# Performance work log

Measured on AMD Instinct MI355X. Metric: run time of the kernel, lower is better.

The kernel has to match this reference:

```python
import jax, jax.numpy as jnp
import numpy as np

DIM = 1024
E = 8
N = 4096
HID = 4 * DIM
THRESHOLD = 0.3


def setup_inputs() -> dict:
    key = jax.random.key(0)
    ks = jax.random.split(key, 8)
    s = 0.02
    return {
        "x": jax.random.normal(ks[0], (N, DIM), dtype=jnp.float32),
        "expert_inputs": jax.random.normal(ks[1], (E, N, DIM), dtype=jnp.float32),
        "wg": jax.random.normal(ks[2], (DIM, E), dtype=jnp.float32) * s,
        "bg": jnp.zeros((E,), dtype=jnp.float32),
        "w1": jax.random.normal(ks[3], (E, DIM, HID), dtype=jnp.float32) * s,
        "b1": jnp.zeros((E, HID), dtype=jnp.float32),
        "w2": jax.random.normal(ks[4], (E, HID, DIM), dtype=jnp.float32) * s,
        "b2": jnp.zeros((E, DIM), dtype=jnp.float32),
    }


def reference(x, expert_inputs, wg, bg, w1, b1, w2, b2):
    # Gate: softmax over experts. [N, E]
    gate_scores = jax.nn.softmax(x @ wg + bg, axis=-1)

    # Experts: FeedForward(dim, dim, mult=4) = Linear -> GELU -> Linear, batched over E.
    h = jax.nn.gelu(jnp.einsum('end,edh->enh', expert_inputs, w1) + b1[:, None, :],
                    approximate=False)  # [E, N, HID]
    expert_outputs = jnp.einsum('enh,ehd->end', h, w2) + b2[:, None, :]  # [E, N, D]
    expert_outputs = jnp.transpose(expert_outputs, (1, 0, 2))  # [N, E, D]

    # Threshold mask + renormalized weighted combine.
    mask = gate_scores >= THRESHOLD
    masked_scores = gate_scores * mask.astype(gate_scores.dtype)
    normed = masked_scores / (masked_scores.sum(axis=1, keepdims=True) + 1e-6)
    fused = jnp.einsum('ne,ned->nd', normed, expert_outputs)  # [N, D]

    # Fallback: rows with no expert above threshold take the top-1 expert output.
    top1 = jnp.argmax(gate_scores, axis=1)  # [N]
    fallback = jnp.take_along_axis(expert_outputs, top1[:, None, None], axis=1)[:, 0, :]
    fb_mask = (mask.sum(axis=1) == 0)[:, None]
    fused = jnp.where(fb_mask, fallback, fused)
    return fused, gate_scores
```

## Files before the change

### kernel.cpp

```cpp
#include <hip/hip_runtime.h>
#include <hip/hip_bf16.h>
#include <cstdint>

#define N_TOK 4096
#define DIM_  1024
#define HID_  4096
#define NEXP  8
#define HHALF 2048
#define CAP   (3 * N_TOK)

typedef __attribute__((ext_vector_type(8))) short short8;
typedef __attribute__((ext_vector_type(4))) float f32x4;

__device__ __forceinline__ unsigned short f32_to_bf16(float f) {
    union { float f; uint32_t u; } v;
    v.f = f;
    uint32_t r = (v.u + 0x7fffu + ((v.u >> 16) & 1u)) >> 16;
    return (unsigned short)r;
}

__device__ __forceinline__ float gelu_exact(float x) {
    return 0.5f * x * (1.0f + erff(x * 0.70710678118654752440f));
}

__device__ __forceinline__ void gl_lds16(const unsigned short* g, unsigned short* l) {
    __builtin_amdgcn_global_load_lds(
        (const __attribute__((address_space(1))) void*)g,
        (__attribute__((address_space(3))) void*)l, 16, 0, 0);
}

__global__ __launch_bounds__(256)
void zero_init_kernel(float* __restrict__ fused, int* __restrict__ cnt)
{
    const int b = blockIdx.x;
    if (b < N_TOK) {
        float4* p = (float4*)(fused + (size_t)b * DIM_);
        const int t = threadIdx.x;
        p[t] = make_float4(0.f, 0.f, 0.f, 0.f);
    } else if (threadIdx.x < NEXP) {
        cnt[threadIdx.x] = 0;
    }
}

__global__ __launch_bounds__(256)
void gate_kernel(const float* __restrict__ x, const float* __restrict__ wg,
                 const float* __restrict__ bg, float* __restrict__ gates,
                 float* __restrict__ wts, int* __restrict__ cnt)
{
    const int n = blockIdx.x;
    const int t = threadIdx.x;
    float acc[NEXP];
#pragma unroll
    for (int e = 0; e < NEXP; e++) acc[e] = 0.0f;
    const float* xr = x + (size_t)n * DIM_;
    for (int k = t; k < DIM_; k += 256) {
        const float xv = xr[k];
        const float* wr = wg + (size_t)k * NEXP;
#pragma unroll
        for (int e = 0; e < NEXP; e++) acc[e] = fmaf(xv, wr[e], acc[e]);
    }
#pragma unroll
    for (int e = 0; e < NEXP; e++) {
#pragma unroll
        for (int off = 32; off > 0; off >>= 1)
            acc[e] += __shfl_down(acc[e], off, 64);
    }
    __shared__ float red[4][NEXP];
    const int lane = t & 63, wave = t >> 6;
    if (lane == 0) {
#pragma unroll
        for (int e = 0; e < NEXP; e++) red[wave][e] = acc[e];
    }
    __syncthreads();
    if (t == 0) {
        float z[NEXP];
#pragma unroll
        for (int e = 0; e < NEXP; e++)
            z[e] = red[0][e] + red[1][e] + red[2][e] + red[3][e] + bg[e];
        float m = z[0];
#pragma unroll
        for (int e = 1; e < NEXP; e++) m = fmaxf(m, z[e]);
        float p[NEXP], s = 0.0f;
#pragma unroll
        for (int e = 0; e < NEXP; e++) { p[e] = __expf(z[e] - m); s += p[e]; }
        const float invs = 1.0f / s;
        float g[NEXP];
        int top = 0;
#pragma unroll
        for (int e = 0; e < NEXP; e++) {
            g[e] = p[e] * invs;
            gates[(size_t)n * NEXP + e] = g[e];
            if (g[e] > g[top]) top = e;
        }
        float w[NEXP], sm = 0.0f;
        int c = 0;
#pragma unroll
        for (int e = 0; e < NEXP; e++) {
            const bool mk = (g[e] >= 0.3f);
            const float ms = mk ? g[e] : 0.0f;
            sm += ms; c += mk ? 1 : 0;
            w[e] = ms;
        }
        if (c == 0) {
#pragma unroll
            for (int e = 0; e < NEXP; e++) w[e] = 0.0f;
            w[top] = 1.0f;
        } else {
            const float inv = 1.0f / (sm + 1e-6f);
#pragma unroll
            for (int e = 0; e < NEXP; e++) w[e] *= inv;
        }
#pragma unroll
        for (int e = 0; e < NEXP; e++) {
            wts[(size_t)n * NEXP + e] = w[e];
            if (w[e] > 0.0f) atomicAdd(&cnt[e], 1);
        }
    }
}

__global__ void offsets_kernel(const int* __restrict__ cnt, int* __restrict__ off,
                               int* __restrict__ cnt2)
{
    if (threadIdx.x == 0) {
        int a = 0;
        for (int e = 0; e < NEXP; e++) { off[e] = a; a += cnt[e]; cnt2[e] = 0; }
    }
}

__global__ __launch_bounds__(256)
void build_list_kernel(const float* __restrict__ wts, const int* __restrict__ off,
                       int* __restrict__ cnt2, int* __restrict__ gidx,
                       float* __restrict__ wpk)
{
    const int n = blockIdx.x * 256 + threadIdx.x;
    if (n >= N_TOK) return;
#pragma unroll
    for (int e = 0; e < NEXP; e++) {
        const float w = wts[(size_t)n * NEXP + e];
        if (w > 0.0f) {
            const int slot = atomicAdd(&cnt2[e], 1);
            const int g = off[e] + slot;
            gidx[g] = n;
            wpk[g] = w;
        }
    }
}

__global__ __launch_bounds__(256)
void gather_cvt_kernel(const float* __restrict__ ei, const int* __restrict__ cnt,
                       const int* __restrict__ off, const int* __restrict__ gidx,
                       unsigned short* __restrict__ xg)
{
    const int e = blockIdx.y;
    const int ne = cnt[e];
    const int i0 = blockIdx.x * 8;
    if (i0 >= ne) return;
    const int grp = threadIdx.x >> 5;
    const int l32 = threadIdx.x & 31;
    const int i = i0 + grp;
    if (i >= ne) return;
    const int o = off[e];
    const float* src = ei + ((size_t)e * N_TOK + gidx[o + i]) * DIM_;
    unsigned short* dst = xg + (size_t)(o + i) * DIM_;
#pragma unroll
    for (int j = 0; j < 8; j++) {
        const int c = (l32 + j * 32) * 4;
        const float4 v = *(const float4*)(src + c);
        ushort4 u;
        u.x = f32_to_bf16(v.x); u.y = f32_to_bf16(v.y);
        u.z = f32_to_bf16(v.z); u.w = f32_to_bf16(v.w);
        *(ushort4*)(dst + c) = u;
    }
}

__global__ __launch_bounds__(256)
void transpose_cvt2(const float* __restrict__ in, unsigned short* __restrict__ out,
                    int R, int C)
{
    __shared__ float tile[64][33];
    const int e  = blockIdx.z;
    const int c0 = blockIdx.x * 32;
    const int r0 = blockIdx.y * 64;
    const int tx = threadIdx.x & 31;
    const int ty = threadIdx.x >> 5;
    const float* src = in + (size_t)e * R * C;
#pragma unroll
    for (int i = 0; i < 8; i++)
        tile[ty + i * 8][tx] = src[(size_t)(r0 + ty + i * 8) * C + (c0 + tx)];
    __syncthreads();
    unsigned short* dst = out + (size_t)e * R * C;
#pragma unroll
    for (int i = 0; i < 4; i++) {
        const int c = ty + i * 8;
        ushort2 p;
        p.x = f32_to_bf16(tile[2 * tx][c]);
        p.y = f32_to_bf16(tile[2 * tx + 1][c]);
        *(ushort2*)&dst[(size_t)(c0 + c) * R + r0 + 2 * tx] = p;
    }
}

__global__ __launch_bounds__(256)
void gemm1_k(const unsigned short* __restrict__ xg, const unsigned short* __restrict__ w1t,
             const float* __restrict__ b1, unsigned short* __restrict__ hg,
             const int* __restrict__ cnt, const int* __restrict__ off, int h0)
{
    const int e = blockIdx.z;
    const int ne = cnt[e];
    const int rowBase = blockIdx.y * 128;
    if (rowBase >= ne) return;
    const int o = off[e];
    const int colBase = blockIdx.x * 128;

    __shared__ __align__(16) unsigned short sA[128 * 32];
    __shared__ __align__(16) unsigned short sB[128 * 32];
    const int tid  = threadIdx.x;
    const int lane = tid & 63;
    const int wave = tid >> 6;
    const int wr = wave >> 1, wc = wave & 1;

    f32x4 acc[4][4];
#pragma unroll
    for (int i = 0; i < 4; i++)
#pragma unroll
        for (int j = 0; j < 4; j++)
#pragma unroll
            for (int r = 0; r < 4; r++) acc[i][j][r] = 0.0f;

    const int sr = tid >> 2;
    const int sc = (tid & 3) << 3;
    const int row0 = min(rowBase + sr, ne - 1);
    const int row1 = min(rowBase + 64 + sr, ne - 1);
    const unsigned short* ga0 = xg + (size_t)(o + row0) * DIM_ + sc;
    const unsigned short* ga1 = xg + (size_t)(o + row1) * DIM_ + sc;
    const unsigned short* gb0 = w1t + ((size_t)e * HID_ + h0 + colBase + sr) * DIM_ + sc;
    const unsigned short* gb1 = gb0 + (size_t)64 * DIM_;
    unsigned short* la0 = sA + tid * 8;
    unsigned short* la1 = sA + 2048 + tid * 8;
    unsigned short* lb0 = sB + tid * 8;
    unsigned short* lb1 = sB + 2048 + tid * 8;

    const int aoff = (wr * 64 + (lane & 15)) * 32 + ((lane >> 4) << 3);
    const int boff = (wc * 64 + (lane & 15)) * 32 + ((lane >> 4) << 3);

    for (int k0 = 0; k0 < DIM_; k0 += 32) {
        gl_lds16(ga0 + k0, la0);
        gl_lds16(ga1 + k0, la1);
        gl_lds16(gb0 + k0, lb0);
        gl_lds16(gb1 + k0, lb1);
        __syncthreads();
        short8 av[4], bv[4];
#pragma unroll
        for (int i = 0; i < 4; i++) av[i] = *(const short8*)(sA + aoff + i * 16 * 32);
#pragma unroll
        for (int j = 0; j < 4; j++) bv[j] = *(const short8*)(sB + boff + j * 16 * 32);
#pragma unroll
        for (int i = 0; i < 4; i++)
#pragma unroll
            for (int j = 0; j < 4; j++)
                acc[i][j] = __builtin_amdgcn_mfma_f32_16x16x32_bf16(av[i], bv[j], acc[i][j], 0, 0, 0);
        __syncthreads();
    }

    const int crow = rowBase + wr * 64 + ((lane >> 4) << 2);
    const int ccol = colBase + wc * 64 + (lane & 15);
#pragma unroll
    for (int i = 0; i < 4; i++) {
#pragma unroll
        for (int j = 0; j < 4; j++) {
            const int col = ccol + j * 16;
            const float b = b1[(size_t)e * HID_ + h0 + col];
#pragma unroll
            for (int r = 0; r < 4; r++) {
                const int row = crow + i * 16 + r;
                if (row < ne) {
                    const float v = acc[i][j][r] + b;
                    hg[(size_t)(o + row) * HHALF + col] = f32_to_bf16(gelu_exact(v));
                }
            }
        }
    }
}

__global__ __launch_bounds__(256)
void gemm2_k(const unsigned short* __restrict__ hg, const unsigned short* __restrict__ w2t,
             const float* __restrict__ b2, float* __restrict__ fused,
             const int* __restrict__ cnt, const int* __restrict__ off,
             const int* __restrict__ gidx, const float* __restrict__ wpk, int h0)
{
    const int e = blockIdx.z;
    const int ne = cnt[e];
    const int rowBase = blockIdx.y * 128;
    if (rowBase >= ne) return;
    const int o = off[e];
    const int colBase = blockIdx.x * 128;

    __shared__ __align__(16) unsigned short sA[128 * 32];
    __shared__ __align__(16) unsigned short sB[128 * 32];
    const int tid  = threadIdx.x;
    const int lane = tid & 63;
    const int wave = tid >> 6;
    const int wr = wave >> 1, wc = wave & 1;

    f32x4 acc[4][4];
#pragma unroll
    for (int i = 0; i < 4; i++)
#pragma unroll
        for (int j = 0; j < 4; j++)
#pragma unroll
            for (int r = 0; r < 4; r++) acc[i][j][r] = 0.0f;

    const int sr = tid >> 2;
    const int sc = (tid & 3) << 3;
    const int row0 = min(rowBase + sr, ne - 1);
    const int row1 = min(rowBase + 64 + sr, ne - 1);
    const unsigned short* ga0 = hg + (size_t)(o + row0) * HHALF + sc;
    const unsigned short* ga1 = hg + (size_t)(o + row1) * HHALF + sc;
    const unsigned short* gb0 = w2t + ((size_t)e * DIM_ + colBase + sr) * HID_ + h0 + sc;
    const unsigned short* gb1 = gb0 + (size_t)64 * HID_;
    unsigned short* la0 = sA + tid * 8;
    unsigned short* la1 = sA + 2048 + tid * 8;
    unsigned short* lb0 = sB + tid * 8;
    unsigned short* lb1 = sB + 2048 + tid * 8;

    const int aoff = (wr * 64 + (lane & 15)) * 32 + ((lane >> 4) << 3);
    const int boff = (wc * 64 + (lane & 15)) * 32 + ((lane >> 4) << 3);

    for (int k0 = 0; k0 < HHALF; k0 += 32) {
        gl_lds16(ga0 + k0, la0);
        gl_lds16(ga1 + k0, la1);
        gl_lds16(gb0 + k0, lb0);
        gl_lds16(gb1 + k0, lb1);
        __syncthreads();
        short8 av[4], bv[4];
#pragma unroll
        for (int i = 0; i < 4; i++) av[i] = *(const short8*)(sA + aoff + i * 16 * 32);
#pragma unroll
        for (int j = 0; j < 4; j++) bv[j] = *(const short8*)(sB + boff + j * 16 * 32);
#pragma unroll
        for (int i = 0; i < 4; i++)
#pragma unroll
            for (int j = 0; j < 4; j++)
                acc[i][j] = __builtin_amdgcn_mfma_f32_16x16x32_bf16(av[i], bv[j], acc[i][j], 0, 0, 0);
        __syncthreads();
    }

    const int crow = rowBase + wr * 64 + ((lane >> 4) << 2);
    const int ccol = colBase + wc * 64 + (lane & 15);
#pragma unroll
    for (int i = 0; i < 4; i++) {
#pragma unroll
        for (int j = 0; j < 4; j++) {
            const int col = ccol + j * 16;
            const float b = (h0 == 0) ? b2[(size_t)e * DIM_ + col] : 0.0f;
#pragma unroll
            for (int r = 0; r < 4; r++) {
                const int row = crow + i * 16 + r;
                if (row < ne) {
                    const float w = wpk[o + row];
                    const int orow = gidx[o + row];
                    atomicAdd(&fused[(size_t)orow * DIM_ + col], w * (acc[i][j][r] + b));
                }
            }
        }
    }
}

extern "C" void kernel_launch(void* const* d_in, const int* in_sizes, int n_in,
                              void* d_out, int out_size, void* d_ws, size_t ws_size,
                              hipStream_t stream)
{
    const float* x  = (const float*)d_in[0];
    const float* ei = (const float*)d_in[1];
    const float* wg = (const float*)d_in[2];
    const float* bg = (const float*)d_in[3];
    const float* w1 = (const float*)d_in[4];
    const float* b1 = (const float*)d_in[5];
    const float* w2 = (const float*)d_in[6];
    const float* b2 = (const float*)d_in[7];

    float* fused = (float*)d_out;
    float* gates = fused + (size_t)N_TOK * DIM_;

    unsigned short* xg  = (unsigned short*)d_ws;
    unsigned short* hg  = xg  + (size_t)CAP * DIM_;
    unsigned short* w1t = hg  + (size_t)CAP * HHALF;
    unsigned short* w2t = w1t + (size_t)NEXP * HID_ * DIM_;
    float* wts = (float*)(w2t + (size_t)NEXP * DIM_ * HID_);
    float* wpk = wts + (size_t)N_TOK * NEXP;
    int* gidx  = (int*)(wpk + CAP);
    int* cnt   = gidx + CAP;
    int* off   = cnt + NEXP;
    int* cnt2  = off + NEXP;

    zero_init_kernel<<<N_TOK + 1, 256, 0, stream>>>(fused, cnt);
    gate_kernel<<<N_TOK, 256, 0, stream>>>(x, wg, bg, gates, wts, cnt);
    offsets_kernel<<<1, 64, 0, stream>>>(cnt, off, cnt2);
    build_list_kernel<<<N_TOK / 256, 256, 0, stream>>>(wts, off, cnt2, gidx, wpk);

    gather_cvt_kernel<<<dim3(N_TOK / 8, NEXP), 256, 0, stream>>>(ei, cnt, off, gidx, xg);
    transpose_cvt2<<<dim3(HID_ / 32, DIM_ / 64, NEXP), 256, 0, stream>>>(w1, w1t, DIM_, HID_);
    transpose_cvt2<<<dim3(DIM_ / 32, HID_ / 64, NEXP), 256, 0, stream>>>(w2, w2t, HID_, DIM_);

    for (int h0 = 0; h0 < HID_; h0 += HHALF) {
        gemm1_k<<<dim3(HHALF / 128, N_TOK / 128, NEXP), 256, 0, stream>>>(
            xg, w1t, b1, hg, cnt, off, h0);
        gemm2_k<<<dim3(DIM_ / 128, N_TOK / 128, NEXP), 256, 0, stream>>>(
            hg, w2t, b2, fused, cnt, off, gidx, wpk, h0);
    }
}
```

Measured before the change: 716.1 us.

## Shrink GEMM row tiles, split-K gemm2, wave-per-token gate, merge weight transposes

Both expert GEMMs now use 64-row tiles instead of 128, and gemm2 adds a two-way split over the hidden dimension. The aim is more blocks, so the GPU stays occupied when per-expert token counts are small or uneven. The gate kernel assigns one token per wavefront with float4 loads and xor shuffles, which removes the shared-memory reduction and block barrier. The two weight transpose launches are merged into one launch. In exchange, the smaller tiles mean less operand reuse per loaded byte, and the split-K doubles the atomic adds into the output.

```diff
diff --git a/kernel.cpp b/kernel.cpp
--- a/kernel.cpp
+++ b/kernel.cpp
@@ -35,8 +35,7 @@
     const int b = blockIdx.x;
     if (b < N_TOK) {
         float4* p = (float4*)(fused + (size_t)b * DIM_);
-        const int t = threadIdx.x;
-        p[t] = make_float4(0.f, 0.f, 0.f, 0.f);
+        p[threadIdx.x] = make_float4(0.f, 0.f, 0.f, 0.f);
     } else if (threadIdx.x < NEXP) {
         cnt[threadIdx.x] = 0;
     }
@@ -47,36 +46,33 @@
                  const float* __restrict__ bg, float* __restrict__ gates,
                  float* __restrict__ wts, int* __restrict__ cnt)
 {
-    const int n = blockIdx.x;
-    const int t = threadIdx.x;
+    const int wave = threadIdx.x >> 6;
+    const int lane = threadIdx.x & 63;
+    const int n = blockIdx.x * 4 + wave;
     float acc[NEXP];
 #pragma unroll
     for (int e = 0; e < NEXP; e++) acc[e] = 0.0f;
-    const float* xr = x + (size_t)n * DIM_;
-    for (int k = t; k < DIM_; k += 256) {
-        const float xv = xr[k];
-        const float* wr = wg + (size_t)k * NEXP;
-#pragma unroll
-        for (int e = 0; e < NEXP; e++) acc[e] = fmaf(xv, wr[e], acc[e]);
+    const float4* xr = (const float4*)(x + (size_t)n * DIM_);
+#pragma unroll
+    for (int j = 0; j < 4; j++) {
+        const int k4 = lane + j * 64;
+        const float4 v = xr[k4];
+        const float* wr = wg + (size_t)k4 * 4 * NEXP;
+#pragma unroll
+        for (int e = 0; e < NEXP; e++)
+            acc[e] += v.x * wr[e] + v.y * wr[NEXP + e] +
+                      v.z * wr[2 * NEXP + e] + v.w * wr[3 * NEXP + e];
     }
 #pragma unroll
     for (int e = 0; e < NEXP; e++) {
 #pragma unroll
         for (int off = 32; off > 0; off >>= 1)
-            acc[e] += __shfl_down(acc[e], off, 64);
-    }
-    __shared__ float red[4][NEXP];
-    const int lane = t & 63, wave = t >> 6;
+            acc[e] += __shfl_xor(acc[e], off, 64);
+    }
     if (lane == 0) {
-#pragma unroll
-        for (int e = 0; e < NEXP; e++) red[wave][e] = acc[e];
-    }
-    __syncthreads();
-    if (t == 0) {
         float z[NEXP];
 #pragma unroll
-        for (int e = 0; e < NEXP; e++)
-            z[e] = red[0][e] + red[1][e] + red[2][e] + red[3][e] + bg[e];
+        for (int e = 0; e < NEXP; e++) z[e] = acc[e] + bg[e];
         float m = z[0];
 #pragma unroll
         for (int e = 1; e < NEXP; e++) m = fmaxf(m, z[e]);
@@ -174,21 +170,33 @@
 }
 
 __global__ __launch_bounds__(256)
-void transpose_cvt2(const float* __restrict__ in, unsigned short* __restrict__ out,
-                    int R, int C)
+void transpose_cvt3(const float* __restrict__ w1, const float* __restrict__ w2,
+                    unsigned short* __restrict__ w1t, unsigned short* __restrict__ w2t)
 {
     __shared__ float tile[64][33];
-    const int e  = blockIdx.z;
-    const int c0 = blockIdx.x * 32;
-    const int r0 = blockIdx.y * 64;
+    const int z = blockIdx.y;
+    const float* src;
+    unsigned short* dst;
+    int cb, rb;
+    if (z < NEXP) {
+        src = w1 + (size_t)z * DIM_ * HID_;
+        dst = w1t + (size_t)z * DIM_ * HID_;
+        cb = blockIdx.x & 127; rb = blockIdx.x >> 7;
+    } else {
+        src = w2 + (size_t)(z - NEXP) * HID_ * DIM_;
+        dst = w2t + (size_t)(z - NEXP) * HID_ * DIM_;
+        cb = blockIdx.x & 31; rb = blockIdx.x >> 5;
+    }
+    const int C = (z < NEXP) ? HID_ : DIM_;
+    const int R = (z < NEXP) ? DIM_ : HID_;
+    const int c0 = cb * 32;
+    const int r0 = rb * 64;
     const int tx = threadIdx.x & 31;
     const int ty = threadIdx.x >> 5;
-    const float* src = in + (size_t)e * R * C;
 #pragma unroll
     for (int i = 0; i < 8; i++)
         tile[ty + i * 8][tx] = src[(size_t)(r0 + ty + i * 8) * C + (c0 + tx)];
     __syncthreads();
-    unsigned short* dst = out + (size_t)e * R * C;
 #pragma unroll
     for (int i = 0; i < 4; i++) {
         const int c = ty + i * 8;
@@ -206,21 +214,21 @@
 {
     const int e = blockIdx.z;
     const int ne = cnt[e];
-    const int rowBase = blockIdx.y * 128;
+    const int rowBase = blockIdx.y * 64;
     if (rowBase >= ne) return;
     const int o = off[e];
     const int colBase = blockIdx.x * 128;
 
-    __shared__ __align__(16) unsigned short sA[128 * 32];
+    __shared__ __align__(16) unsigned short sA[64 * 32];
     __shared__ __align__(16) unsigned short sB[128 * 32];
     const int tid  = threadIdx.x;
     const int lane = tid & 63;
     const int wave = tid >> 6;
     const int wr = wave >> 1, wc = wave & 1;
 
-    f32x4 acc[4][4];
-#pragma unroll
-    for (int i = 0; i < 4; i++)
+    f32x4 acc[2][4];
+#pragma unroll
+    for (int i = 0; i < 2; i++)
 #pragma unroll
         for (int j = 0; j < 4; j++)
 #pragma unroll
@@ -228,43 +236,39 @@
 
     const int sr = tid >> 2;
     const int sc = (tid & 3) << 3;
-    const int row0 = min(rowBase + sr, ne - 1);
-    const int row1 = min(rowBase + 64 + sr, ne - 1);
-    const unsigned short* ga0 = xg + (size_t)(o + row0) * DIM_ + sc;
-    const unsigned short* ga1 = xg + (size_t)(o + row1) * DIM_ + sc;
+    const int rowA = min(rowBase + sr, ne - 1);
+    const unsigned short* ga0 = xg + (size_t)(o + rowA) * DIM_ + sc;
     const unsigned short* gb0 = w1t + ((size_t)e * HID_ + h0 + colBase + sr) * DIM_ + sc;
     const unsigned short* gb1 = gb0 + (size_t)64 * DIM_;
     unsigned short* la0 = sA + tid * 8;
-    unsigned short* la1 = sA + 2048 + tid * 8;
     unsigned short* lb0 = sB + tid * 8;
     unsigned short* lb1 = sB + 2048 + tid * 8;
 
-    const int aoff = (wr * 64 + (lane & 15)) * 32 + ((lane >> 4) << 3);
+    const int aoff = (wr * 32 + (lane & 15)) * 32 + ((lane >> 4) << 3);
     const int boff = (wc * 64 + (lane & 15)) * 32 + ((lane >> 4) << 3);
 
     for (int k0 = 0; k0 < DIM_; k0 += 32) {
         gl_lds16(ga0 + k0, la0);
-        gl_lds16(ga1 + k0, la1);
         gl_lds16(gb0 + k0, lb0);
         gl_lds16(gb1 + k0, lb1);
         __syncthreads();
-        short8 av[4], bv[4];
-#pragma unroll
-        for (int i = 0; i < 4; i++) av[i] = *(const short8*)(sA + aoff + i * 16 * 32);
+        short8 av[2], bv[4];
+#pragma unroll
+        for (int i = 0; i < 2; i++) av[i] = *(const short8*)(sA + aoff + i * 16 * 32);
 #pragma unroll
         for (int j = 0; j < 4; j++) bv[j] = *(const short8*)(sB + boff + j * 16 * 32);
 #pragma unroll
-        for (int i = 0; i < 4; i++)
+        for (int i = 0; i < 2; i++)
 #pragma unroll
             for (int j = 0; j < 4; j++)
                 acc[i][j] = __builtin_amdgcn_mfma_f32_16x16x32_bf16(av[i], bv[j], acc[i][j], 0, 0, 0);
         __syncthreads();
     }
 
-    const int crow = rowBase + wr * 64 + ((lane >> 4) << 2);
+    const int crow = rowBase + wr * 32 + ((lane >> 4) << 2);
     const int ccol = colBase + wc * 64 + (lane & 15);
 #pragma unroll
-    for (int i = 0; i < 4; i++) {
+    for (int i = 0; i < 2; i++) {
 #pragma unroll
         for (int j = 0; j < 4; j++) {
             const int col = ccol + j * 16;
@@ -289,21 +293,23 @@
 {
     const int e = blockIdx.z;
     const int ne = cnt[e];
-    const int rowBase = blockIdx.y * 128;
+    const int rowBase = blockIdx.y * 64;
     if (rowBase >= ne) return;
     const int o = off[e];
-    const int colBase = blockIdx.x * 128;
-
-    __shared__ __align__(16) unsigned short sA[128 * 32];
+    const int colBase = (blockIdx.x & 7) * 128;
+    const int kc = blockIdx.x >> 3;
+    const int kbeg = kc * (HHALF / 2);
+
+    __shared__ __align__(16) unsigned short sA[64 * 32];
     __shared__ __align__(16) unsigned short sB[128 * 32];
     const int tid  = threadIdx.x;
     const int lane = tid & 63;
     const int wave = tid >> 6;
     const int wr = wave >> 1, wc = wave & 1;
 
-    f32x4 acc[4][4];
-#pragma unroll
-    for (int i = 0; i < 4; i++)
+    f32x4 acc[2][4];
+#pragma unroll
+    for (int i = 0; i < 2; i++)
 #pragma unroll
         for (int j = 0; j < 4; j++)
 #pragma unroll
@@ -311,47 +317,44 @@
 
     const int sr = tid >> 2;
     const int sc = (tid & 3) << 3;
-    const int row0 = min(rowBase + sr, ne - 1);
-    const int row1 = min(rowBase + 64 + sr, ne - 1);
-    const unsigned short* ga0 = hg + (size_t)(o + row0) * HHALF + sc;
-    const unsigned short* ga1 = hg + (size_t)(o + row1) * HHALF + sc;
-    const unsigned short* gb0 = w2t + ((size_t)e * DIM_ + colBase + sr) * HID_ + h0 + sc;
+    const int rowA = min(rowBase + sr, ne - 1);
+    const unsigned short* ga0 = hg + (size_t)(o + rowA) * HHALF + kbeg + sc;
+    const unsigned short* gb0 = w2t + ((size_t)e * DIM_ + colBase + sr) * HID_ + h0 + kbeg + sc;
     const unsigned short* gb1 = gb0 + (size_t)64 * HID_;
     unsigned short* la0 = sA + tid * 8;
-    unsigned short* la1 = sA + 2048 + tid * 8;
     unsigned short* lb0 = sB + tid * 8;
     unsigned short* lb1 = sB + 2048 + tid * 8;
 
-    const int aoff = (wr * 64 + (lane & 15)) * 32 + ((lane >> 4) << 3);
+    const int aoff = (wr * 32 + (lane & 15)) * 32 + ((lane >> 4) << 3);
     const int boff = (wc * 64 + (lane & 15)) * 32 + ((lane >> 4) << 3);
 
-    for (int k0 = 0; k0 < HHALF; k0 += 32) {
+    for (int k0 = 0; k0 < HHALF / 2; k0 += 32) {
         gl_lds16(ga0 + k0, la0);
-        gl_lds16(ga1 + k0, la1);
         gl_lds16(gb0 + k0, lb0);
         gl_lds16(gb1 + k0, lb1);
         __syncthreads();
-        short8 av[4], bv[4];
-#pragma unroll
-        for (int i = 0; i < 4; i++) av[i] = *(const short8*)(sA + aoff + i * 16 * 32);
+        short8 av[2], bv[4];
+#pragma unroll
+        for (int i = 0; i < 2; i++) av[i] = *(const short8*)(sA + aoff + i * 16 * 32);
 #pragma unroll
         for (int j = 0; j < 4; j++) bv[j] = *(const short8*)(sB + boff + j * 16 * 32);
 #pragma unroll
-        for (int i = 0; i < 4; i++)
+        for (int i = 0; i < 2; i++)
 #pragma unroll
             for (int j = 0; j < 4; j++)
                 acc[i][j] = __builtin_amdgcn_mfma_f32_16x16x32_bf16(av[i], bv[j], acc[i][j], 0, 0, 0);
         __syncthreads();
     }
 
-    const int crow = rowBase + wr * 64 + ((lane >> 4) << 2);
+    const int crow = rowBase + wr * 32 + ((lane >> 4) << 2);
     const int ccol = colBase + wc * 64 + (lane & 15);
-#pragma unroll
-    for (int i = 0; i < 4; i++) {
+    const int addBias = (h0 == 0 && kc == 0);
+#pragma unroll
+    for (int i = 0; i < 2; i++) {
 #pragma unroll
         for (int j = 0; j < 4; j++) {
             const int col = ccol + j * 16;
-            const float b = (h0 == 0) ? b2[(size_t)e * DIM_ + col] : 0.0f;
+            const float b = addBias ? b2[(size_t)e * DIM_ + col] : 0.0f;
 #pragma unroll
             for (int r = 0; r < 4; r++) {
                 const int row = crow + i * 16 + r;
@@ -393,18 +396,17 @@
     int* cnt2  = off + NEXP;
 
     zero_init_kernel<<<N_TOK + 1, 256, 0, stream>>>(fused, cnt);
-    gate_kernel<<<N_TOK, 256, 0, stream>>>(x, wg, bg, gates, wts, cnt);
+    gate_kernel<<<N_TOK / 4, 256, 0, stream>>>(x, wg, bg, gates, wts, cnt);
     offsets_kernel<<<1, 64, 0, stream>>>(cnt, off, cnt2);
     build_list_kernel<<<N_TOK / 256, 256, 0, stream>>>(wts, off, cnt2, gidx, wpk);
 
     gather_cvt_kernel<<<dim3(N_TOK / 8, NEXP), 256, 0, stream>>>(ei, cnt, off, gidx, xg);
-    transpose_cvt2<<<dim3(HID_ / 32, DIM_ / 64, NEXP), 256, 0, stream>>>(w1, w1t, DIM_, HID_);
-    transpose_cvt2<<<dim3(DIM_ / 32, HID_ / 64, NEXP), 256, 0, stream>>>(w2, w2t, HID_, DIM_);
+    transpose_cvt3<<<dim3(2048, 16), 256, 0, stream>>>(w1, w2, w1t, w2t);
 
     for (int h0 = 0; h0 < HID_; h0 += HHALF) {
-        gemm1_k<<<dim3(HHALF / 128, N_TOK / 128, NEXP), 256, 0, stream>>>(
+        gemm1_k<<<dim3(HHALF / 128, N_TOK / 64, NEXP), 256, 0, stream>>>(
             xg, w1t, b1, hg, cnt, off, h0);
-        gemm2_k<<<dim3(DIM_ / 128, N_TOK / 128, NEXP), 256, 0, stream>>>(
+        gemm2_k<<<dim3(16, N_TOK / 64, NEXP), 256, 0, stream>>>(
             hg, w2t, b2, fused, cnt, off, gidx, wpk, h0);
     }
 }
```

After: 670.5 us. 6.4% less time.
